# Kernel tuning notes

Measured on AMD Instinct MI355X. Metric: run time of the kernel, lower is better.

The kernel has to match this reference:

```python
import jax, jax.numpy as jnp
import numpy as np

N = 200000   # num_nodes
D = 64       # embedding_dims
B = 4096     # batch of target nodes (batched per-edge processing)
K = 128      # padded in-neighbor count per target
W = 20       # window_size (history deque length)
H = 128      # hidden_size


def setup_inputs() -> dict:
    key = jax.random.key(0)
    ks = jax.random.split(key, 14)
    return {
        "adj_time": jax.random.uniform(ks[0], (N,), jnp.float32),          # last-seen times in [0,1)
        "gc": jax.random.uniform(ks[1], (N,), jnp.float32),                 # per-node centrality scalar (dict_gc)
        "cur_time": jnp.ones((1,), jnp.float32),                            # current event time (>= all stored times)
        "neigh_mask": jnp.ones((B, K), jnp.float32),                        # 1 = valid neighbor slot
        "hist_feat": jax.random.normal(ks[2], (B, W, 2 * D), jnp.float32),  # feature_dict[...]['feature'] deque
        "hist_time": jax.random.uniform(ks[3], (B, W), jnp.float32),        # feature_dict[...]['time'] deque
        "t2v_w": jax.random.normal(ks[4], (D,), jnp.float32),               # Time2Vec('cos') weights
        "t2v_b": jax.random.normal(ks[5], (D,), jnp.float32),
        "node_w": jax.random.normal(ks[6], (D,), jnp.float32),              # linear_node: Linear(1, D)
        "node_b": jax.random.normal(ks[7], (D,), jnp.float32),
        "att_w": jax.random.normal(ks[8], (2 * D,), jnp.float32),           # Attention: score = cat(a,b) @ w + b
        "att_b": jax.random.normal(ks[9], (1,), jnp.float32),
        "weight": jax.random.normal(ks[10], (H, 4 * D), jnp.float32) * 0.05,
        "targets": jax.random.randint(ks[11], (B,), 0, N),
        "neigh_idx": jax.random.randint(ks[12], (B, K), 0, N),
    }


def reference(adj_time, gc, cur_time, neigh_mask, hist_feat, hist_time,
              t2v_w, t2v_b, node_w, node_b, att_w, att_b, weight,
              targets, neigh_idx):
    t = cur_time[0]

    def node_encoding(idx):
        # Time2Vec('cos'): first channel linear, rest cos(w*dt+b)
        dt = jnp.abs(t - adj_time[idx])[..., None]            # [..., 1]
        phase = t2v_w * dt + t2v_b                            # [..., D]
        tv = jnp.concatenate([phase[..., :1], jnp.cos(phase[..., 1:])], axis=-1)
        feat = jax.nn.relu(tv + gc[idx][..., None] * node_w + node_b)
        # F.normalize (L2 over feature dim)
        return feat / jnp.maximum(jnp.linalg.norm(feat, axis=-1, keepdims=True), 1e-12)

    tgt_feat = node_encoding(targets)       # [B, D]
    ngh_feat = node_encoding(neigh_idx)     # [B, K, D]

    # Decayer(2, 'log'): time_score = 1 / (2 * log(e + dt))
    time_score = 1.0 / (2.0 * jnp.log(jnp.e + (t - adj_time[neigh_idx])))   # [B, K]
    # Attention score between target and each neighbor encoding
    att = (tgt_feat @ att_w[:D])[:, None] \
        + jnp.einsum("bkd,d->bk", ngh_feat, att_w[D:]) + att_b[0]           # [B, K]
    score = jax.nn.leaky_relu(time_score + att, 0.01) * neigh_mask          # [B, K]
    neigh_agg = jnp.einsum("bk,bkd->bd", score, ngh_feat)                   # [B, D]

    combined = jnp.concatenate([tgt_feat, neigh_agg], axis=-1)              # [B, 2D]

    # History aggregation with Decayer(2, 'rev'): w = 1 / (2 * (1 + dt))
    hist_w = 1.0 / (2.0 * (1.0 + (t - hist_time)))                          # [B, W]
    hist_agg = jnp.einsum("bw,bwd->bd", hist_w, hist_feat)                  # [B, 2D]

    feat4 = jnp.concatenate([hist_agg, combined], axis=-1)                  # [B, 4D]
    return jax.nn.relu(feat4 @ weight.T)                                    # [B, H]
```

## Files before the change

kernel.cpp:

```cpp
#include <hip/hip_runtime.h>
#include <math.h>

#define NN 200000
#define DD 64
#define BB 4096
#define KK 128
#define WW 20
#define HH 128

__device__ __forceinline__ float fast_rcp(float x) { return __builtin_amdgcn_rcpf(x); }
__device__ __forceinline__ float fast_rsq(float x) { return __builtin_amdgcn_rsqf(x); }

__global__ __launch_bounds__(256) void k1_encode(
    const float* __restrict__ adj_time, const float* __restrict__ gc,
    const float* __restrict__ cur_time, const float* __restrict__ neigh_mask,
    const float* __restrict__ hist_feat, const float* __restrict__ hist_time,
    const float* __restrict__ t2v_w, const float* __restrict__ t2v_b,
    const float* __restrict__ node_w, const float* __restrict__ node_b,
    const float* __restrict__ att_w, const float* __restrict__ att_b,
    const int* __restrict__ targets, const int* __restrict__ neigh_idx,
    float* __restrict__ feat4)
{
    const int b    = blockIdx.x;
    const int tid  = threadIdx.x;
    const int lane = tid & 63;
    const int wid  = tid >> 6;
    const int k    = tid & 127;
    const int half = tid >> 7;

    __shared__ float  hws[WW];
    __shared__ float  hpart[128];
    __shared__ float4 dtg[128];
    __shared__ float2 sp[2][128];
    __shared__ float  aggp[4][64];
    __shared__ float  stL;

    const float t = cur_time[0];

    float ts_k = 0.f, m_k = 0.f;
    if (tid < 128) {
        int   idx = neigh_idx[b * KK + k];
        m_k       = neigh_mask[b * KK + k];
        float at  = adj_time[idx];
        float g   = gc[idx];
        float dt  = fabsf(t - at);
        dtg[k]    = make_float4(dt, g, 0.f, 0.f);
        ts_k      = fast_rcp(2.0f * __logf(2.71828182845904523536f + (t - at)));
    } else if (wid == 2) {
        if (lane < WW)
            hws[lane] = fast_rcp(2.0f * (1.0f + (t - hist_time[b * WW + lane])));
    } else {
        int   tg  = targets[b];
        float dtT = fabsf(t - adj_time[tg]);
        float gT  = gc[tg];
        float pw  = t2v_w[lane], pb = t2v_b[lane];
        float nw  = node_w[lane], nb2 = node_b[lane];
        float ph  = fmaf(pw, dtT, pb);
        float tv  = (lane == 0) ? ph : __cosf(ph);
        float f   = fmaxf(tv + fmaf(gT, nw, nb2), 0.f);
        float ss  = f * f;
#pragma unroll
        for (int off = 32; off; off >>= 1) ss += __shfl_xor(ss, off, 64);
        float invn = fast_rsq(fmaxf(ss, 1e-24f));
        float tfn  = f * invn;
        float sdt  = tfn * att_w[lane];
#pragma unroll
        for (int off = 32; off; off >>= 1) sdt += __shfl_xor(sdt, off, 64);
        if (lane == 0) stL = sdt;
        feat4[b * 256 + 128 + lane] = tfn;
    }
    __syncthreads();

    float hv[10];
    {
        const float* hf = hist_feat + (size_t)b * WW * 128 + (tid & 127);
#pragma unroll
        for (int w = 0; w < 10; ++w) hv[w] = hf[(half * 10 + w) * 128];
    }

    {
        const int d0 = half * 32;
        float4 dg = dtg[k];
        float  dt = dg.x, g = dg.y;
        float  s2 = 0.f, sd = 0.f;
#pragma unroll
        for (int dd = 0; dd < 32; ++dd) {
            int   d   = d0 + dd;
            float pw  = t2v_w[d], pb = t2v_b[d];
            float nw  = node_w[d], nb2 = node_b[d];
            float a2  = att_w[64 + d];
            float ph  = fmaf(pw, dt, pb);
            float cv  = __cosf(ph);
            float tv  = (d == 0) ? ph : cv;
            float f   = fmaxf(tv + fmaf(g, nw, nb2), 0.f);
            s2 = fmaf(f, f, s2);
            sd = fmaf(f, a2, sd);
        }
        sp[half][k] = make_float2(s2, sd);
    }

    float hsum = 0.f;
#pragma unroll
    for (int w = 0; w < 10; ++w) hsum = fmaf(hws[half * 10 + w], hv[w], hsum);
    if (half) hpart[tid & 127] = hsum;

    __syncthreads();

    if (!half) {
        feat4[b * 256 + (tid & 127)] = hsum + hpart[tid & 127];
        float2 a0 = sp[0][k], a1 = sp[1][k];
        float  s2 = a0.x + a1.x;
        float  sd = a0.y + a1.y;
        float  invn = fast_rsq(fmaxf(s2, 1e-24f));
        float  sc = ts_k + stL + sd * invn + att_b[0];
        sc = (sc > 0.f) ? sc : 0.01f * sc;
        dtg[k].z = sc * m_k * invn;
    }
    __syncthreads();

    {
        float pw  = t2v_w[lane], pb = t2v_b[lane];
        float nw  = node_w[lane], nb2 = node_b[lane];
        float acc = 0.f;
        const int k0 = wid * 32;
#pragma unroll 8
        for (int j = 0; j < 32; ++j) {
            float4 dg = dtg[k0 + j];
            float  ph = fmaf(pw, dg.x, pb);
            float  cv = __cosf(ph);
            float  tv = (lane == 0) ? ph : cv;
            float  f  = fmaxf(tv + fmaf(dg.y, nw, nb2), 0.f);
            acc = fmaf(dg.z, f, acc);
        }
        aggp[wid][lane] = acc;
    }
    __syncthreads();

    if (tid < 64) {
        feat4[b * 256 + 192 + tid] =
            aggp[0][tid] + aggp[1][tid] + aggp[2][tid] + aggp[3][tid];
    }
}

__global__ __launch_bounds__(256) void k2_gemm(
    const float* __restrict__ feat4, const float* __restrict__ weight,
    float* __restrict__ out)
{
    const int b0  = blockIdx.x * 8;
    const int tid = threadIdx.x;

    __shared__ float tile[8 * 256];
    __shared__ float wl[128 * 33];

    {
        const float4* src = (const float4*)(feat4 + (size_t)b0 * 256);
        float4* dst = (float4*)tile;
        dst[tid]       = src[tid];
        dst[tid + 256] = src[tid + 256];
    }

    const int h = tid & 127;
    const int g = tid >> 7;
    const float* tb = tile + (g * 4) * 256;

    float acc0 = 0.f, acc1 = 0.f, acc2 = 0.f, acc3 = 0.f;

    for (int c = 0; c < 8; ++c) {
        __syncthreads();
#pragma unroll
        for (int i = 0; i < 16; ++i) {
            int l  = i * 256 + tid;
            int hh = l >> 5;
            int jj = l & 31;
            wl[hh * 33 + jj] = weight[hh * 256 + c * 32 + jj];
        }
        __syncthreads();

#pragma unroll
        for (int jj = 0; jj < 32; jj += 4) {
            float w0 = wl[h * 33 + jj + 0];
            float w1 = wl[h * 33 + jj + 1];
            float w2 = wl[h * 33 + jj + 2];
            float w3 = wl[h * 33 + jj + 3];
            float4 f0 = *(const float4*)(tb + 0 * 256 + c * 32 + jj);
            float4 f1 = *(const float4*)(tb + 1 * 256 + c * 32 + jj);
            float4 f2 = *(const float4*)(tb + 2 * 256 + c * 32 + jj);
            float4 f3 = *(const float4*)(tb + 3 * 256 + c * 32 + jj);
            acc0 += w0 * f0.x + w1 * f0.y + w2 * f0.z + w3 * f0.w;
            acc1 += w0 * f1.x + w1 * f1.y + w2 * f1.z + w3 * f1.w;
            acc2 += w0 * f2.x + w1 * f2.y + w2 * f2.z + w3 * f2.w;
            acc3 += w0 * f3.x + w1 * f3.y + w2 * f3.z + w3 * f3.w;
        }
    }

    out[(size_t)(b0 + g * 4 + 0) * 128 + h] = fmaxf(acc0, 0.f);
    out[(size_t)(b0 + g * 4 + 1) * 128 + h] = fmaxf(acc1, 0.f);
    out[(size_t)(b0 + g * 4 + 2) * 128 + h] = fmaxf(acc2, 0.f);
    out[(size_t)(b0 + g * 4 + 3) * 128 + h] = fmaxf(acc3, 0.f);
}

extern "C" void kernel_launch(void* const* d_in, const int* in_sizes, int n_in,
                              void* d_out, int out_size, void* d_ws, size_t ws_size,
                              hipStream_t stream) {
    const float* adj_time  = (const float*)d_in[0];
    const float* gc        = (const float*)d_in[1];
    const float* cur_time  = (const float*)d_in[2];
    const float* neigh_mask= (const float*)d_in[3];
    const float* hist_feat = (const float*)d_in[4];
    const float* hist_time = (const float*)d_in[5];
    const float* t2v_w     = (const float*)d_in[6];
    const float* t2v_b     = (const float*)d_in[7];
    const float* node_w    = (const float*)d_in[8];
    const float* node_b    = (const float*)d_in[9];
    const float* att_w     = (const float*)d_in[10];
    const float* att_b     = (const float*)d_in[11];
    const float* weight    = (const float*)d_in[12];
    const int*   targets   = (const int*)d_in[13];
    const int*   neigh_idx = (const int*)d_in[14];

    float* out   = (float*)d_out;
    float* feat4 = (float*)d_ws;

    k1_encode<<<BB, 256, 0, stream>>>(adj_time, gc, cur_time, neigh_mask,
                                      hist_feat, hist_time, t2v_w, t2v_b,
                                      node_w, node_b, att_w, att_b,
                                      targets, neigh_idx, feat4);

    k2_gemm<<<BB / 8, 256, 0, stream>>>(feat4, weight, out);
}
```

Measured before the change: 144.3 us.

## Fuse encoding and output GEMM into one kernel processing eight rows per block

Merges the per-target encoding kernel and the dense output projection into a single 512-thread kernel that handles 8 batch rows per block and keeps the 256-wide feature rows in shared memory. This removes the workspace round trip for feat4 and one kernel launch. Work is also redistributed: each thread computes full 64-dim neighbor norms and scores for two slots, and each wave aggregates all 128 neighbors for one row, which drops the partial-sum exchanges. The trade-offs are a grid of 512 blocks instead of 4096, more shared memory per block, and the weight matrix being reloaded per 8-row block inside a kernel that also does the encoding work.

```diff
diff --git a/kernel.cpp b/kernel.cpp
--- a/kernel.cpp
+++ b/kernel.cpp
@@ -7,57 +7,59 @@
 #define KK 128
 #define WW 20
 #define HH 128
+#define TPB 512
+#define RPB 8
 
 __device__ __forceinline__ float fast_rcp(float x) { return __builtin_amdgcn_rcpf(x); }
 __device__ __forceinline__ float fast_rsq(float x) { return __builtin_amdgcn_rsqf(x); }
 
-__global__ __launch_bounds__(256) void k1_encode(
+__global__ __launch_bounds__(512, 4) void fused(
     const float* __restrict__ adj_time, const float* __restrict__ gc,
     const float* __restrict__ cur_time, const float* __restrict__ neigh_mask,
     const float* __restrict__ hist_feat, const float* __restrict__ hist_time,
     const float* __restrict__ t2v_w, const float* __restrict__ t2v_b,
     const float* __restrict__ node_w, const float* __restrict__ node_b,
     const float* __restrict__ att_w, const float* __restrict__ att_b,
+    const float* __restrict__ weight,
     const int* __restrict__ targets, const int* __restrict__ neigh_idx,
-    float* __restrict__ feat4)
+    float* __restrict__ out)
 {
-    const int b    = blockIdx.x;
+    const int b0   = blockIdx.x * RPB;
     const int tid  = threadIdx.x;
     const int lane = tid & 63;
-    const int wid  = tid >> 6;
-    const int k    = tid & 127;
-    const int half = tid >> 7;
+    const int wv   = tid >> 6;
 
-    __shared__ float  hws[WW];
-    __shared__ float  hpart[128];
-    __shared__ float4 dtg[128];
-    __shared__ float2 sp[2][128];
-    __shared__ float  aggp[4][64];
-    __shared__ float  stL;
+    __shared__ float2 dtg[RPB * KK];
+    __shared__ float  wk[RPB * KK];
+    __shared__ float  hws[RPB][WW];
+    __shared__ float  stL[RPB];
+    __shared__ float  tile[RPB * 256];
+    __shared__ float  wl[128 * 33];
 
     const float t = cur_time[0];
 
-    float ts_k = 0.f, m_k = 0.f;
-    if (tid < 128) {
-        int   idx = neigh_idx[b * KK + k];
-        m_k       = neigh_mask[b * KK + k];
-        float at  = adj_time[idx];
-        float g   = gc[idx];
-        float dt  = fabsf(t - at);
-        dtg[k]    = make_float4(dt, g, 0.f, 0.f);
-        ts_k      = fast_rcp(2.0f * __logf(2.71828182845904523536f + (t - at)));
-    } else if (wid == 2) {
-        if (lane < WW)
-            hws[lane] = fast_rcp(2.0f * (1.0f + (t - hist_time[b * WW + lane])));
-    } else {
-        int   tg  = targets[b];
+    float ts_r[2], m_r[2];
+#pragma unroll
+    for (int i = 0; i < 2; ++i) {
+        int   slot = tid + i * TPB;
+        int   idx  = neigh_idx[b0 * KK + slot];
+        m_r[i]     = neigh_mask[b0 * KK + slot];
+        float at   = adj_time[idx];
+        float g    = gc[idx];
+        dtg[slot]  = make_float2(fabsf(t - at), g);
+        ts_r[i]    = fast_rcp(2.0f * __logf(2.71828182845904523536f + (t - at)));
+    }
+    if (tid < RPB * WW) {
+        int r = tid / WW, w = tid - r * WW;
+        hws[r][w] = fast_rcp(2.0f * (1.0f + (t - hist_time[(b0 + r) * WW + w])));
+    }
+    {
+        int   tg  = targets[b0 + wv];
         float dtT = fabsf(t - adj_time[tg]);
         float gT  = gc[tg];
-        float pw  = t2v_w[lane], pb = t2v_b[lane];
-        float nw  = node_w[lane], nb2 = node_b[lane];
-        float ph  = fmaf(pw, dtT, pb);
-        float tv  = (lane == 0) ? ph : __cosf(ph);
-        float f   = fmaxf(tv + fmaf(gT, nw, nb2), 0.f);
+        float ph  = fmaf(t2v_w[lane], dtT, t2v_b[lane]);
+        float tv_ = (lane == 0) ? ph : __cosf(ph);
+        float f   = fmaxf(tv_ + fmaf(gT, node_w[lane], node_b[lane]), 0.f);
         float ss  = f * f;
 #pragma unroll
         for (int off = 32; off; off >>= 1) ss += __shfl_xor(ss, off, 64);
@@ -66,112 +68,74 @@
         float sdt  = tfn * att_w[lane];
 #pragma unroll
         for (int off = 32; off; off >>= 1) sdt += __shfl_xor(sdt, off, 64);
-        if (lane == 0) stL = sdt;
-        feat4[b * 256 + 128 + lane] = tfn;
+        if (lane == 0) stL[wv] = sdt;
+        tile[wv * 256 + 128 + lane] = tfn;
     }
     __syncthreads();
 
-    float hv[10];
-    {
-        const float* hf = hist_feat + (size_t)b * WW * 128 + (tid & 127);
+    const float ab = att_b[0];
 #pragma unroll
-        for (int w = 0; w < 10; ++w) hv[w] = hf[(half * 10 + w) * 128];
+    for (int i = 0; i < 2; ++i) {
+        int    slot = tid + i * TPB;
+        int    r    = slot >> 7;
+        float2 dg   = dtg[slot];
+        float  s2 = 0.f, sd = 0.f;
+#pragma unroll 8
+        for (int d = 0; d < 64; ++d) {
+            float ph  = fmaf(t2v_w[d], dg.x, t2v_b[d]);
+            float cv  = __cosf(ph);
+            float tv_ = (d == 0) ? ph : cv;
+            float f   = fmaxf(tv_ + fmaf(dg.y, node_w[d], node_b[d]), 0.f);
+            s2 = fmaf(f, f, s2);
+            sd = fmaf(f, att_w[64 + d], sd);
+        }
+        float invn = fast_rsq(fmaxf(s2, 1e-24f));
+        float sc   = ts_r[i] + stL[r] + sd * invn + ab;
+        sc = (sc > 0.f) ? sc : 0.01f * sc;
+        wk[slot] = sc * m_r[i] * invn;
     }
 
-    {
-        const int d0 = half * 32;
-        float4 dg = dtg[k];
-        float  dt = dg.x, g = dg.y;
-        float  s2 = 0.f, sd = 0.f;
 #pragma unroll
-        for (int dd = 0; dd < 32; ++dd) {
-            int   d   = d0 + dd;
-            float pw  = t2v_w[d], pb = t2v_b[d];
-            float nw  = node_w[d], nb2 = node_b[d];
-            float a2  = att_w[64 + d];
-            float ph  = fmaf(pw, dt, pb);
-            float cv  = __cosf(ph);
-            float tv  = (d == 0) ? ph : cv;
-            float f   = fmaxf(tv + fmaf(g, nw, nb2), 0.f);
-            s2 = fmaf(f, f, s2);
-            sd = fmaf(f, a2, sd);
-        }
-        sp[half][k] = make_float2(s2, sd);
-    }
-
-    float hsum = 0.f;
+    for (int i = 0; i < 2; ++i) {
+        int col = tid + i * TPB;
+        int r = col >> 7, d = col & 127;
+        const float* hf = hist_feat + (size_t)(b0 + r) * WW * 128 + d;
+        float s = 0.f;
 #pragma unroll
-    for (int w = 0; w < 10; ++w) hsum = fmaf(hws[half * 10 + w], hv[w], hsum);
-    if (half) hpart[tid & 127] = hsum;
-
-    __syncthreads();
-
-    if (!half) {
-        feat4[b * 256 + (tid & 127)] = hsum + hpart[tid & 127];
-        float2 a0 = sp[0][k], a1 = sp[1][k];
-        float  s2 = a0.x + a1.x;
-        float  sd = a0.y + a1.y;
-        float  invn = fast_rsq(fmaxf(s2, 1e-24f));
-        float  sc = ts_k + stL + sd * invn + att_b[0];
-        sc = (sc > 0.f) ? sc : 0.01f * sc;
-        dtg[k].z = sc * m_k * invn;
+        for (int w = 0; w < WW; ++w) s = fmaf(hws[r][w], hf[w * 128], s);
+        tile[r * 256 + d] = s;
     }
     __syncthreads();
 
     {
-        float pw  = t2v_w[lane], pb = t2v_b[lane];
-        float nw  = node_w[lane], nb2 = node_b[lane];
+        float pw = t2v_w[lane], pb = t2v_b[lane];
+        float nw = node_w[lane], nb2 = node_b[lane];
         float acc = 0.f;
-        const int k0 = wid * 32;
+        const int base = wv * KK;
 #pragma unroll 8
-        for (int j = 0; j < 32; ++j) {
-            float4 dg = dtg[k0 + j];
+        for (int k = 0; k < KK; ++k) {
+            float2 dg = dtg[base + k];
+            float  w_ = wk[base + k];
             float  ph = fmaf(pw, dg.x, pb);
             float  cv = __cosf(ph);
-            float  tv = (lane == 0) ? ph : cv;
-            float  f  = fmaxf(tv + fmaf(dg.y, nw, nb2), 0.f);
-            acc = fmaf(dg.z, f, acc);
+            float  tv_ = (lane == 0) ? ph : cv;
+            float  f  = fmaxf(tv_ + fmaf(dg.y, nw, nb2), 0.f);
+            acc = fmaf(w_, f, acc);
         }
-        aggp[wid][lane] = acc;
-    }
-    __syncthreads();
-
-    if (tid < 64) {
-        feat4[b * 256 + 192 + tid] =
-            aggp[0][tid] + aggp[1][tid] + aggp[2][tid] + aggp[3][tid];
-    }
-}
-
-__global__ __launch_bounds__(256) void k2_gemm(
-    const float* __restrict__ feat4, const float* __restrict__ weight,
-    float* __restrict__ out)
-{
-    const int b0  = blockIdx.x * 8;
-    const int tid = threadIdx.x;
-
-    __shared__ float tile[8 * 256];
-    __shared__ float wl[128 * 33];
-
-    {
-        const float4* src = (const float4*)(feat4 + (size_t)b0 * 256);
-        float4* dst = (float4*)tile;
-        dst[tid]       = src[tid];
-        dst[tid + 256] = src[tid + 256];
+        tile[wv * 256 + 192 + lane] = acc;
     }
 
     const int h = tid & 127;
     const int g = tid >> 7;
-    const float* tb = tile + (g * 4) * 256;
-
-    float acc0 = 0.f, acc1 = 0.f, acc2 = 0.f, acc3 = 0.f;
+    const float* tb = tile + (g * 2) * 256;
+    float acc0 = 0.f, acc1 = 0.f;
 
     for (int c = 0; c < 8; ++c) {
         __syncthreads();
 #pragma unroll
-        for (int i = 0; i < 16; ++i) {
-            int l  = i * 256 + tid;
-            int hh = l >> 5;
-            int jj = l & 31;
+        for (int i = 0; i < 8; ++i) {
+            int l  = i * TPB + tid;
+            int hh = l >> 5, jj = l & 31;
             wl[hh * 33 + jj] = weight[hh * 256 + c * 32 + jj];
         }
         __syncthreads();
@@ -184,19 +148,13 @@
             float w3 = wl[h * 33 + jj + 3];
             float4 f0 = *(const float4*)(tb + 0 * 256 + c * 32 + jj);
             float4 f1 = *(const float4*)(tb + 1 * 256 + c * 32 + jj);
-            float4 f2 = *(const float4*)(tb + 2 * 256 + c * 32 + jj);
-            float4 f3 = *(const float4*)(tb + 3 * 256 + c * 32 + jj);
             acc0 += w0 * f0.x + w1 * f0.y + w2 * f0.z + w3 * f0.w;
             acc1 += w0 * f1.x + w1 * f1.y + w2 * f1.z + w3 * f1.w;
-            acc2 += w0 * f2.x + w1 * f2.y + w2 * f2.z + w3 * f2.w;
-            acc3 += w0 * f3.x + w1 * f3.y + w2 * f3.z + w3 * f3.w;
         }
     }
 
-    out[(size_t)(b0 + g * 4 + 0) * 128 + h] = fmaxf(acc0, 0.f);
-    out[(size_t)(b0 + g * 4 + 1) * 128 + h] = fmaxf(acc1, 0.f);
-    out[(size_t)(b0 + g * 4 + 2) * 128 + h] = fmaxf(acc2, 0.f);
-    out[(size_t)(b0 + g * 4 + 3) * 128 + h] = fmaxf(acc3, 0.f);
+    out[(size_t)(b0 + g * 2 + 0) * 128 + h] = fmaxf(acc0, 0.f);
+    out[(size_t)(b0 + g * 2 + 1) * 128 + h] = fmaxf(acc1, 0.f);
 }
 
 extern "C" void kernel_launch(void* const* d_in, const int* in_sizes, int n_in,
@@ -218,13 +176,10 @@
     const int*   targets   = (const int*)d_in[13];
     const int*   neigh_idx = (const int*)d_in[14];
 
-    float* out   = (float*)d_out;
-    float* feat4 = (float*)d_ws;
+    float* out = (float*)d_out;
 
-    k1_encode<<<BB, 256, 0, stream>>>(adj_time, gc, cur_time, neigh_mask,
-                                      hist_feat, hist_time, t2v_w, t2v_b,
-                                      node_w, node_b, att_w, att_b,
-                                      targets, neigh_idx, feat4);
-
-    k2_gemm<<<BB / 8, 256, 0, stream>>>(feat4, weight, out);
+    fused<<<BB / RPB, TPB, 0, stream>>>(adj_time, gc, cur_time, neigh_mask,
+                                        hist_feat, hist_time, t2v_w, t2v_b,
+                                        node_w, node_b, att_w, att_b, weight,
+                                        targets, neigh_idx, out);
 }
```

Measured after the change: 135.6 us. 1.06x faster.
